# Kernel optimization log

Hardware: AMD Instinct MI355X
Metric: run time of the kernel (lower is better)

The kernel has to match this reference:

```python
import jax, jax.numpy as jnp
import numpy as np

# norse default LIF/LI parameters
DT = 0.001
TAU_SYN_INV = 200.0
TAU_MEM_INV = 100.0
V_TH = 1.0
ALPHA = 100.0        # SuperSpike surrogate slope (method='super', alpha=100)
T_ENC = 40           # ConstantCurrentLIFEncoder(40)
SCALE = 50.0

STATE_DIM = 256
ACTIONS = 18
HIDDEN = 128
BATCH = 1024

@jax.custom_vjp
def spike(x):
    return (x > 0).astype(x.dtype)

def _spike_fwd(x):
    return spike(x), x

def _spike_bwd(x, g):
    # SuperSpike surrogate: 1 / (alpha*|x| + 1)^2
    return (g / (ALPHA * jnp.abs(x) + 1.0) ** 2,)

spike.defvjp(_spike_fwd, _spike_bwd)

def encode(current):
    # constant-current LIF encoder: current [B, D] -> spikes [T_ENC, B, D]
    def step(v, _):
        v = v + DT * TAU_MEM_INV * (-v + current)   # v_leak = 0
        z = spike(v - V_TH)
        v = (1.0 - z) * v                            # reset to v_reset = 0
        return v, z
    _, zs = jax.lax.scan(step, jnp.zeros_like(current), None, length=T_ENC)
    return zs

def snn_forward(x, w_in, w_rec, w_actor, w_critic):
    # encode positive and negative rectified currents, concat on feature dim
    xs = jnp.concatenate([encode(jax.nn.relu(SCALE * x)),
                          encode(jax.nn.relu(-SCALE * x))], axis=2)  # [T, B, 2D]
    B = x.shape[0]
    H = w_in.shape[0]
    A = w_actor.shape[0]
    dt_ = x.dtype
    carry0 = (jnp.zeros((B, H), dt_), jnp.zeros((B, H), dt_), jnp.zeros((B, H), dt_),
              jnp.zeros((B, A), dt_), jnp.zeros((B, A), dt_),
              jnp.zeros((B, 1), dt_), jnp.zeros((B, 1), dt_))

    def step(carry, x_t):
        z, v, i, va, ia, vc, ic = carry
        # --- recurrent LIFCell (norse lif_step) ---
        v_dec = v + DT * TAU_MEM_INV * (-v + i)      # dv uses pre-decay i
        i_dec = i - DT * TAU_SYN_INV * i
        z_new = spike(v_dec - V_TH)
        v_new = (1.0 - z_new) * v_dec                # reset by z to v_reset = 0
        i_new = i_dec + x_t @ w_in.T + z @ w_rec.T   # recurrent input uses old z
        # --- LICell actor readout (norse li_step) ---
        va_new = va + DT * TAU_MEM_INV * (-va + ia)
        ia_new = ia - DT * TAU_SYN_INV * ia + z_new @ w_actor.T
        # --- LICell critic readout ---
        vc_new = vc + DT * TAU_MEM_INV * (-vc + ic)
        ic_new = ic - DT * TAU_SYN_INV * ic + z_new @ w_critic.T
        return (z_new, v_new, i_new, va_new, ia_new, vc_new, ic_new), (va_new, vc_new)

    _, (volt_a, volt_c) = jax.lax.scan(step, carry0, xs)
    m_a = jnp.max(volt_a, axis=0)                    # max over time
    m_c = jnp.max(volt_c, axis=0)
    return jax.nn.softmax(m_a, axis=1), m_c


def setup_inputs() -> dict:
    key = jax.random.key(0)
    k0, k1, k2, k3, k4 = jax.random.split(key, 5)
    in_feat = 2 * STATE_DIM
    x = jax.random.normal(k0, (BATCH, STATE_DIM), dtype=jnp.float32)
    # norse init: randn * sqrt(2 / input_size)
    w_in = jax.random.normal(k1, (HIDDEN, in_feat), dtype=jnp.float32) * np.sqrt(2.0 / in_feat)
    w_rec = jax.random.normal(k2, (HIDDEN, HIDDEN), dtype=jnp.float32) * np.sqrt(2.0 / HIDDEN)
    w_actor = jax.random.normal(k3, (ACTIONS, HIDDEN), dtype=jnp.float32) * np.sqrt(2.0 / HIDDEN)
    w_critic = jax.random.normal(k4, (1, HIDDEN), dtype=jnp.float32) * np.sqrt(2.0 / HIDDEN)
    return {"x": x, "w_in": w_in, "w_rec": w_rec, "w_actor": w_actor, "w_critic": w_critic}


def reference(x, w_in, w_rec, w_actor, w_critic):
    return snn_forward(x, w_in, w_rec, w_actor, w_critic)
```

## Files before the change

kernel.cpp:

```cpp
#include <hip/hip_runtime.h>
#include <hip/hip_bf16.h>
#include <stdint.h>

typedef __attribute__((ext_vector_type(4))) float f32x4;
typedef __attribute__((ext_vector_type(8))) short s16x8;
typedef __attribute__((ext_vector_type(4))) unsigned int u32x4;

#define OFF_I 2621440

__device__ __forceinline__ void lut_entry(uint32_t by, uint32_t* r) {
    uint32_t r0 = 0, r1 = 0, r2 = 0, r3 = 0;
    if (by & 1)   r0 |= 0x3F80u;
    if (by & 2)   r0 |= 0x3F800000u;
    if (by & 4)   r1 |= 0x3F80u;
    if (by & 8)   r1 |= 0x3F800000u;
    if (by & 16)  r2 |= 0x3F80u;
    if (by & 32)  r2 |= 0x3F800000u;
    if (by & 64)  r3 |= 0x3F80u;
    if (by & 128) r3 |= 0x3F800000u;
    r[0] = r0; r[1] = r1; r[2] = r2; r[3] = r3;
}

__global__ __launch_bounds__(256) void k_encode(const float* __restrict__ x,
                                                uint32_t* __restrict__ spk) {
    int gid  = blockIdx.x * 256 + threadIdx.x;
    int b    = gid >> 9;
    int f    = gid & 511;
    int lane = threadIdx.x & 63;
    float xv  = x[b * 256 + (f & 255)];
    float cur = (f < 256) ? fmaxf(50.f * xv, 0.f) : fmaxf(-50.f * xv, 0.f);
    int wbase = (f >> 6) << 1;
    float v = 0.f;
    for (int t = 0; t < 40; ++t) {
        v = v + 0.1f * (cur - v);
        bool z = (v - 1.0f) > 0.f;
        unsigned long long m = __ballot(z);
        if (z) v = 0.f;
        if (lane == 0)
            *(unsigned long long*)&spk[(size_t)(t * 1024 + b) * 16 + wbase] = m;
    }
}

__global__ __launch_bounds__(512, 1) void k_ingemm(const uint32_t* __restrict__ spk,
                                                   const float* __restrict__ w_in,
                                                   float* __restrict__ I) {
    __shared__ uint32_t lut[256][4];
    __shared__ float tile[16][128];
    const int tid = threadIdx.x;
    if (tid < 256) lut_entry(tid, lut[tid]);
    const int lane = tid & 63, wid = tid >> 6;
    const int fr = lane & 15, fo = lane >> 4;
    const int n0 = wid * 16;

#define LOADB(i) s16x8 bh##i, bl##i; { \
    const float* p = w_in + (n0 + fr) * 512 + (i) * 32 + fo * 8; \
    f32x4 fa = *(const f32x4*)p; f32x4 fb = *(const f32x4*)(p + 4); \
    _Pragma("unroll") for (int j = 0; j < 8; ++j) { \
        float f = (j < 4) ? fa[j] : fb[j - 4]; \
        __hip_bfloat16 hb = __float2bfloat16(f); \
        float r1 = f - __bfloat162float(hb); \
        __hip_bfloat16 lb = __float2bfloat16(r1); \
        bh##i[j] = (short)*(unsigned short*)&hb; \
        bl##i[j] = (short)*(unsigned short*)&lb; } }
    LOADB(0)  LOADB(1)  LOADB(2)  LOADB(3)  LOADB(4)  LOADB(5)  LOADB(6)  LOADB(7)
    LOADB(8)  LOADB(9)  LOADB(10) LOADB(11) LOADB(12) LOADB(13) LOADB(14) LOADB(15)
#undef LOADB
    asm volatile("" : "+v"(bh0), "+v"(bh1), "+v"(bh2),  "+v"(bh3),
                      "+v"(bh4), "+v"(bh5), "+v"(bh6),  "+v"(bh7),
                      "+v"(bh8), "+v"(bh9), "+v"(bh10), "+v"(bh11),
                      "+v"(bh12),"+v"(bh13),"+v"(bh14), "+v"(bh15));
    asm volatile("" : "+v"(bl0), "+v"(bl1), "+v"(bl2),  "+v"(bl3),
                      "+v"(bl4), "+v"(bl5), "+v"(bl6),  "+v"(bl7),
                      "+v"(bl8), "+v"(bl9), "+v"(bl10), "+v"(bl11),
                      "+v"(bl12),"+v"(bl13),"+v"(bl14), "+v"(bl15));
    __syncthreads();

    const int m0 = blockIdx.x * 160;
    const int srow = tid >> 5;
    const int sc0  = (tid & 31) * 4;
    for (int mt = 0; mt < 10; ++mt) {
        int mrow = m0 + mt * 16 + fr;
        u32x4 w0 = *(const u32x4*)&spk[mrow * 16];
        u32x4 w1 = *(const u32x4*)&spk[mrow * 16 + 4];
        u32x4 w2 = *(const u32x4*)&spk[mrow * 16 + 8];
        u32x4 w3 = *(const u32x4*)&spk[mrow * 16 + 12];
        f32x4 acc = (f32x4)0.f;
#define KSTEP(i, WSEL) { uint32_t by = ((WSEL) >> (fo * 8)) & 0xFFu; \
        union { u32x4 u; s16x8 v; } cv; cv.u = *(const u32x4*)lut[by]; \
        acc = __builtin_amdgcn_mfma_f32_16x16x32_bf16(cv.v, bh##i, acc, 0, 0, 0); \
        acc = __builtin_amdgcn_mfma_f32_16x16x32_bf16(cv.v, bl##i, acc, 0, 0, 0); }
        KSTEP(0,  w0[0]) KSTEP(1,  w0[1]) KSTEP(2,  w0[2]) KSTEP(3,  w0[3])
        KSTEP(4,  w1[0]) KSTEP(5,  w1[1]) KSTEP(6,  w1[2]) KSTEP(7,  w1[3])
        KSTEP(8,  w2[0]) KSTEP(9,  w2[1]) KSTEP(10, w2[2]) KSTEP(11, w2[3])
        KSTEP(12, w3[0]) KSTEP(13, w3[1]) KSTEP(14, w3[2]) KSTEP(15, w3[3])
#undef KSTEP
        __syncthreads();
#pragma unroll
        for (int r = 0; r < 4; ++r)
            tile[fo * 4 + r][n0 + fr] = acc[r];
        __syncthreads();
        f32x4 vv = *(const f32x4*)&tile[srow][sc0];
        *(f32x4*)&I[(size_t)(m0 + mt * 16 + srow) * 128 + sc0] = vv;
    }
}

__global__ __launch_bounds__(256, 1) void k_recur_ro(const float* __restrict__ I,
                                                     const float* __restrict__ w_rec,
                                                     const float* __restrict__ w_actor,
                                                     const float* __restrict__ w_critic,
                                                     float* __restrict__ out) {
    __shared__ uint32_t lut[256][4];
    __shared__ uint32_t zm[2][16][4];
    __shared__ float smax[16][20];
    const int tid = threadIdx.x;
    lut_entry(tid, lut[tid]);
    if (tid < 64) zm[0][tid >> 2][tid & 3] = 0;
    const int lane = tid & 63, w = tid >> 6;
    const int fr = lane & 15, fo = lane >> 4;
    const int n0 = w * 32;
    const int b0 = blockIdx.x * 16;

#define LOADW(ks, ni) s16x8 H##ks##ni, L##ks##ni, Q##ks##ni; { \
    const float* p = w_rec + (n0 + (ni) * 16 + fr) * 128 + (ks) * 32 + fo * 8; \
    _Pragma("unroll") for (int j = 0; j < 8; ++j) { \
        float f = p[j]; \
        __hip_bfloat16 hb = __float2bfloat16(f); \
        float r1 = f - __bfloat162float(hb); \
        __hip_bfloat16 lb = __float2bfloat16(r1); \
        float r2 = r1 - __bfloat162float(lb); \
        __hip_bfloat16 qb = __float2bfloat16(r2); \
        H##ks##ni[j] = (short)*(unsigned short*)&hb; \
        L##ks##ni[j] = (short)*(unsigned short*)&lb; \
        Q##ks##ni[j] = (short)*(unsigned short*)&qb; } }
    LOADW(0,0) LOADW(1,0) LOADW(2,0) LOADW(3,0)
    LOADW(0,1) LOADW(1,1) LOADW(2,1) LOADW(3,1)
#undef LOADW
    asm volatile("" : "+v"(H00), "+v"(H10), "+v"(H20), "+v"(H30),
                      "+v"(H01), "+v"(H11), "+v"(H21), "+v"(H31),
                      "+v"(L00), "+v"(L10), "+v"(L20), "+v"(L30));
    asm volatile("" : "+v"(L01), "+v"(L11), "+v"(L21), "+v"(L31),
                      "+v"(Q00), "+v"(Q10), "+v"(Q20), "+v"(Q30),
                      "+v"(Q01), "+v"(Q11), "+v"(Q21), "+v"(Q31));

    s16x8 rbh[4], rbl[4];
    const int a_ch = w * 16 + fr;
    const float* asrc = (a_ch < 18) ? (w_actor + a_ch * 128)
                       : ((a_ch == 18) ? w_critic : nullptr);
#pragma unroll
    for (int ks = 0; ks < 4; ++ks) {
#pragma unroll
        for (int j = 0; j < 8; ++j) {
            float f = asrc ? asrc[ks * 32 + fo * 8 + j] : 0.f;
            __hip_bfloat16 hb = __float2bfloat16(f);
            float r1 = f - __bfloat162float(hb);
            __hip_bfloat16 lb = __float2bfloat16(r1);
            rbh[ks][j] = (short)*(unsigned short*)&hb;
            rbl[ks][j] = (short)*(unsigned short*)&lb;
        }
    }
    f32x4 rva = (f32x4)0.f, ria = (f32x4)0.f, rma = (f32x4)(-1e30f);

    f32x4 v0 = (f32x4)0.f, v1 = (f32x4)0.f, c0 = (f32x4)0.f, c1 = (f32x4)0.f;

#define ILOAD(dst, t_, ni) { _Pragma("unroll") for (int r = 0; r < 4; ++r) \
    dst[r] = I[(size_t)((t_) * 1024 + b0 + fo * 4 + r) * 128 + n0 + (ni) * 16 + fr]; }
    f32x4 icur0, icur1;
    ILOAD(icur0, 0, 0) ILOAD(icur1, 0, 1)
    __syncthreads();

    for (int t = 0; t < 40; ++t) {
        int tn = (t < 39) ? t + 1 : 39;
        f32x4 inxt0, inxt1;
        ILOAD(inxt0, tn, 0) ILOAD(inxt1, tn, 1)

        u32x4 zw = *(const u32x4*)zm[t & 1][fr];
        union { u32x4 u; s16x8 v; } a0, a1, a2, a3;
        a0.u = *(const u32x4*)lut[(zw[0] >> (fo * 8)) & 0xFFu];
        a1.u = *(const u32x4*)lut[(zw[1] >> (fo * 8)) & 0xFFu];
        a2.u = *(const u32x4*)lut[(zw[2] >> (fo * 8)) & 0xFFu];
        a3.u = *(const u32x4*)lut[(zw[3] >> (fo * 8)) & 0xFFu];

        f32x4 r0 = (f32x4)0.f, r1 = (f32x4)0.f;
#define RECK(ks, av) \
        r0 = __builtin_amdgcn_mfma_f32_16x16x32_bf16(av, H##ks##0, r0, 0, 0, 0); \
        r0 = __builtin_amdgcn_mfma_f32_16x16x32_bf16(av, L##ks##0, r0, 0, 0, 0); \
        r0 = __builtin_amdgcn_mfma_f32_16x16x32_bf16(av, Q##ks##0, r0, 0, 0, 0); \
        r1 = __builtin_amdgcn_mfma_f32_16x16x32_bf16(av, H##ks##1, r1, 0, 0, 0); \
        r1 = __builtin_amdgcn_mfma_f32_16x16x32_bf16(av, L##ks##1, r1, 0, 0, 0); \
        r1 = __builtin_amdgcn_mfma_f32_16x16x32_bf16(av, Q##ks##1, r1, 0, 0, 0);
        RECK(0, a0.v) RECK(1, a1.v) RECK(2, a2.v) RECK(3, a3.v)
#undef RECK

        f32x4 vd0 = v0 + 0.1f * (c0 - v0);
        f32x4 vd1 = v1 + 0.1f * (c1 - v1);
        f32x4 id0 = c0 - 0.2f * c0;
        f32x4 id1 = c1 - 0.2f * c1;
        unsigned long long B00, B01, B02, B03, B10, B11, B12, B13;
        bool z;
        z = (vd0[0] - 1.0f) > 0.f; B00 = __ballot(z); if (z) vd0[0] = 0.f;
        z = (vd0[1] - 1.0f) > 0.f; B01 = __ballot(z); if (z) vd0[1] = 0.f;
        z = (vd0[2] - 1.0f) > 0.f; B02 = __ballot(z); if (z) vd0[2] = 0.f;
        z = (vd0[3] - 1.0f) > 0.f; B03 = __ballot(z); if (z) vd0[3] = 0.f;
        z = (vd1[0] - 1.0f) > 0.f; B10 = __ballot(z); if (z) vd1[0] = 0.f;
        z = (vd1[1] - 1.0f) > 0.f; B11 = __ballot(z); if (z) vd1[1] = 0.f;
        z = (vd1[2] - 1.0f) > 0.f; B12 = __ballot(z); if (z) vd1[2] = 0.f;
        z = (vd1[3] - 1.0f) > 0.f; B13 = __ballot(z); if (z) vd1[3] = 0.f;
        v0 = vd0; v1 = vd1;

        if (lane < 16) {
            int m = lane, rq = m & 3, sh = (m >> 2) * 16;
            unsigned long long s0 = (rq == 0) ? B00 : (rq == 1) ? B01 : (rq == 2) ? B02 : B03;
            unsigned long long s1 = (rq == 0) ? B10 : (rq == 1) ? B11 : (rq == 2) ? B12 : B13;
            uint32_t word = ((uint32_t)(s0 >> sh) & 0xFFFFu)
                          | (((uint32_t)(s1 >> sh) & 0xFFFFu) << 16);
            zm[(t & 1) ^ 1][m][w] = word;
        }

        c0 = (id0 + icur0) + r0;
        c1 = (id1 + icur1) + r1;
        icur0 = inxt0; icur1 = inxt1;
        __syncthreads();

        if (w < 2) {
            u32x4 zw2 = *(const u32x4*)zm[(t & 1) ^ 1][fr];
            f32x4 racc = (f32x4)0.f;
#pragma unroll
            for (int ks = 0; ks < 4; ++ks) {
                uint32_t by = (zw2[ks] >> (fo * 8)) & 0xFFu;
                union { u32x4 u; s16x8 v; } cv;
                cv.u = *(const u32x4*)lut[by];
                racc = __builtin_amdgcn_mfma_f32_16x16x32_bf16(cv.v, rbh[ks], racc, 0, 0, 0);
                racc = __builtin_amdgcn_mfma_f32_16x16x32_bf16(cv.v, rbl[ks], racc, 0, 0, 0);
            }
            f32x4 nva = rva + 0.1f * (ria - rva);
            ria = ria - 0.2f * ria + racc;
            rva = nva;
#pragma unroll
            for (int r = 0; r < 4; ++r)
                rma[r] = fmaxf(rma[r], nva[r]);
        }
    }
#undef ILOAD

    if (w == 0) {
#pragma unroll
        for (int r = 0; r < 4; ++r) smax[fo * 4 + r][fr] = rma[r];
    } else if (w == 1 && fr < 3) {
#pragma unroll
        for (int r = 0; r < 4; ++r) smax[fo * 4 + r][16 + fr] = rma[r];
    }
    __syncthreads();
    if (tid < 16) {
        int row = tid;
        float mx = -1e30f;
#pragma unroll
        for (int a2 = 0; a2 < 18; ++a2) mx = fmaxf(mx, smax[row][a2]);
        float s = 0.f;
#pragma unroll
        for (int a2 = 0; a2 < 18; ++a2) s += expf(smax[row][a2] - mx);
#pragma unroll
        for (int a2 = 0; a2 < 18; ++a2)
            out[(b0 + row) * 18 + a2] = expf(smax[row][a2] - mx) / s;
        out[18432 + b0 + row] = smax[row][18];
    }
}

extern "C" void kernel_launch(void* const* d_in, const int* in_sizes, int n_in,
                              void* d_out, int out_size, void* d_ws, size_t ws_size,
                              hipStream_t stream) {
    const float* x        = (const float*)d_in[0];
    const float* w_in     = (const float*)d_in[1];
    const float* w_rec    = (const float*)d_in[2];
    const float* w_actor  = (const float*)d_in[3];
    const float* w_critic = (const float*)d_in[4];
    float* out = (float*)d_out;
    char* ws = (char*)d_ws;
    uint32_t* spk = (uint32_t*)ws;
    float*    I   = (float*)(ws + OFF_I);

    hipLaunchKernelGGL(k_encode,   dim3(2048), dim3(256), 0, stream, x, spk);
    hipLaunchKernelGGL(k_ingemm,   dim3(256),  dim3(512), 0, stream, spk, w_in, I);
    hipLaunchKernelGGL(k_recur_ro, dim3(64),   dim3(256), 0, stream,
                       I, w_rec, w_actor, w_critic, out);
}
```

Baseline: 135.0 us.

## Split recurrent kernel across 8 waves with 16 hidden columns each

The recurrent LIF kernel now runs 512 threads per block, so each of eight waves owns 16 hidden neurons instead of 32. This halves the serial MFMA chain per wave on each time step. The spike bitmask moves to 16-bit words laid out so the existing 4x32-bit read still sees the same bytes. It adds barrier cost for more waves and relies on the new packing matching the old word layout.

```diff
diff --git a/kernel.cpp b/kernel.cpp
--- a/kernel.cpp
+++ b/kernel.cpp
@@ -104,24 +104,24 @@
     }
 }
 
-__global__ __launch_bounds__(256, 1) void k_recur_ro(const float* __restrict__ I,
+__global__ __launch_bounds__(512, 1) void k_recur_ro(const float* __restrict__ I,
                                                      const float* __restrict__ w_rec,
                                                      const float* __restrict__ w_actor,
                                                      const float* __restrict__ w_critic,
                                                      float* __restrict__ out) {
     __shared__ uint32_t lut[256][4];
-    __shared__ uint32_t zm[2][16][4];
+    __shared__ __align__(16) uint16_t zm16[2][16][8];
     __shared__ float smax[16][20];
     const int tid = threadIdx.x;
-    lut_entry(tid, lut[tid]);
-    if (tid < 64) zm[0][tid >> 2][tid & 3] = 0;
+    if (tid < 256) lut_entry(tid, lut[tid]);
+    if (tid < 128) ((uint16_t*)zm16)[tid] = 0;
     const int lane = tid & 63, w = tid >> 6;
     const int fr = lane & 15, fo = lane >> 4;
-    const int n0 = w * 32;
+    const int n0 = w * 16;
     const int b0 = blockIdx.x * 16;
 
-#define LOADW(ks, ni) s16x8 H##ks##ni, L##ks##ni, Q##ks##ni; { \
-    const float* p = w_rec + (n0 + (ni) * 16 + fr) * 128 + (ks) * 32 + fo * 8; \
+#define LOADW(ks) s16x8 H##ks, L##ks, Q##ks; { \
+    const float* p = w_rec + (n0 + fr) * 128 + (ks) * 32 + fo * 8; \
     _Pragma("unroll") for (int j = 0; j < 8; ++j) { \
         float f = p[j]; \
         __hip_bfloat16 hb = __float2bfloat16(f); \
@@ -129,23 +129,20 @@
         __hip_bfloat16 lb = __float2bfloat16(r1); \
         float r2 = r1 - __bfloat162float(lb); \
         __hip_bfloat16 qb = __float2bfloat16(r2); \
-        H##ks##ni[j] = (short)*(unsigned short*)&hb; \
-        L##ks##ni[j] = (short)*(unsigned short*)&lb; \
-        Q##ks##ni[j] = (short)*(unsigned short*)&qb; } }
-    LOADW(0,0) LOADW(1,0) LOADW(2,0) LOADW(3,0)
-    LOADW(0,1) LOADW(1,1) LOADW(2,1) LOADW(3,1)
+        H##ks[j] = (short)*(unsigned short*)&hb; \
+        L##ks[j] = (short)*(unsigned short*)&lb; \
+        Q##ks[j] = (short)*(unsigned short*)&qb; } }
+    LOADW(0) LOADW(1) LOADW(2) LOADW(3)
 #undef LOADW
-    asm volatile("" : "+v"(H00), "+v"(H10), "+v"(H20), "+v"(H30),
-                      "+v"(H01), "+v"(H11), "+v"(H21), "+v"(H31),
-                      "+v"(L00), "+v"(L10), "+v"(L20), "+v"(L30));
-    asm volatile("" : "+v"(L01), "+v"(L11), "+v"(L21), "+v"(L31),
-                      "+v"(Q00), "+v"(Q10), "+v"(Q20), "+v"(Q30),
-                      "+v"(Q01), "+v"(Q11), "+v"(Q21), "+v"(Q31));
+    asm volatile("" : "+v"(H0), "+v"(H1), "+v"(H2), "+v"(H3),
+                      "+v"(L0), "+v"(L1), "+v"(L2), "+v"(L3),
+                      "+v"(Q0), "+v"(Q1), "+v"(Q2), "+v"(Q3));
 
     s16x8 rbh[4], rbl[4];
     const int a_ch = w * 16 + fr;
-    const float* asrc = (a_ch < 18) ? (w_actor + a_ch * 128)
-                       : ((a_ch == 18) ? w_critic : nullptr);
+    const float* asrc = (w < 2)
+        ? ((a_ch < 18) ? (w_actor + a_ch * 128) : ((a_ch == 18) ? w_critic : nullptr))
+        : nullptr;
 #pragma unroll
     for (int ks = 0; ks < 4; ++ks) {
 #pragma unroll
@@ -160,69 +157,56 @@
     }
     f32x4 rva = (f32x4)0.f, ria = (f32x4)0.f, rma = (f32x4)(-1e30f);
 
-    f32x4 v0 = (f32x4)0.f, v1 = (f32x4)0.f, c0 = (f32x4)0.f, c1 = (f32x4)0.f;
-
-#define ILOAD(dst, t_, ni) { _Pragma("unroll") for (int r = 0; r < 4; ++r) \
-    dst[r] = I[(size_t)((t_) * 1024 + b0 + fo * 4 + r) * 128 + n0 + (ni) * 16 + fr]; }
-    f32x4 icur0, icur1;
-    ILOAD(icur0, 0, 0) ILOAD(icur1, 0, 1)
+    f32x4 v0 = (f32x4)0.f, c0 = (f32x4)0.f;
+
+#define ILOAD(dst, t_) { _Pragma("unroll") for (int r = 0; r < 4; ++r) \
+    dst[r] = I[(size_t)((t_) * 1024 + b0 + fo * 4 + r) * 128 + n0 + fr]; }
+    f32x4 icur;
+    ILOAD(icur, 0)
     __syncthreads();
 
     for (int t = 0; t < 40; ++t) {
         int tn = (t < 39) ? t + 1 : 39;
-        f32x4 inxt0, inxt1;
-        ILOAD(inxt0, tn, 0) ILOAD(inxt1, tn, 1)
-
-        u32x4 zw = *(const u32x4*)zm[t & 1][fr];
+        f32x4 inxt;
+        ILOAD(inxt, tn)
+
+        u32x4 zw = *(const u32x4*)zm16[t & 1][fr];
         union { u32x4 u; s16x8 v; } a0, a1, a2, a3;
         a0.u = *(const u32x4*)lut[(zw[0] >> (fo * 8)) & 0xFFu];
         a1.u = *(const u32x4*)lut[(zw[1] >> (fo * 8)) & 0xFFu];
         a2.u = *(const u32x4*)lut[(zw[2] >> (fo * 8)) & 0xFFu];
         a3.u = *(const u32x4*)lut[(zw[3] >> (fo * 8)) & 0xFFu];
 
-        f32x4 r0 = (f32x4)0.f, r1 = (f32x4)0.f;
+        f32x4 r0 = (f32x4)0.f;
 #define RECK(ks, av) \
-        r0 = __builtin_amdgcn_mfma_f32_16x16x32_bf16(av, H##ks##0, r0, 0, 0, 0); \
-        r0 = __builtin_amdgcn_mfma_f32_16x16x32_bf16(av, L##ks##0, r0, 0, 0, 0); \
-        r0 = __builtin_amdgcn_mfma_f32_16x16x32_bf16(av, Q##ks##0, r0, 0, 0, 0); \
-        r1 = __builtin_amdgcn_mfma_f32_16x16x32_bf16(av, H##ks##1, r1, 0, 0, 0); \
-        r1 = __builtin_amdgcn_mfma_f32_16x16x32_bf16(av, L##ks##1, r1, 0, 0, 0); \
-        r1 = __builtin_amdgcn_mfma_f32_16x16x32_bf16(av, Q##ks##1, r1, 0, 0, 0);
+        r0 = __builtin_amdgcn_mfma_f32_16x16x32_bf16(av, H##ks, r0, 0, 0, 0); \
+        r0 = __builtin_amdgcn_mfma_f32_16x16x32_bf16(av, L##ks, r0, 0, 0, 0); \
+        r0 = __builtin_amdgcn_mfma_f32_16x16x32_bf16(av, Q##ks, r0, 0, 0, 0);
         RECK(0, a0.v) RECK(1, a1.v) RECK(2, a2.v) RECK(3, a3.v)
 #undef RECK
 
-        f32x4 vd0 = v0 + 0.1f * (c0 - v0);
-        f32x4 vd1 = v1 + 0.1f * (c1 - v1);
-        f32x4 id0 = c0 - 0.2f * c0;
-        f32x4 id1 = c1 - 0.2f * c1;
-        unsigned long long B00, B01, B02, B03, B10, B11, B12, B13;
+        f32x4 vd = v0 + 0.1f * (c0 - v0);
+        f32x4 id = c0 - 0.2f * c0;
+        unsigned long long B0, B1, B2, B3;
         bool z;
-        z = (vd0[0] - 1.0f) > 0.f; B00 = __ballot(z); if (z) vd0[0] = 0.f;
-        z = (vd0[1] - 1.0f) > 0.f; B01 = __ballot(z); if (z) vd0[1] = 0.f;
-        z = (vd0[2] - 1.0f) > 0.f; B02 = __ballot(z); if (z) vd0[2] = 0.f;
-        z = (vd0[3] - 1.0f) > 0.f; B03 = __ballot(z); if (z) vd0[3] = 0.f;
-        z = (vd1[0] - 1.0f) > 0.f; B10 = __ballot(z); if (z) vd1[0] = 0.f;
-        z = (vd1[1] - 1.0f) > 0.f; B11 = __ballot(z); if (z) vd1[1] = 0.f;
-        z = (vd1[2] - 1.0f) > 0.f; B12 = __ballot(z); if (z) vd1[2] = 0.f;
-        z = (vd1[3] - 1.0f) > 0.f; B13 = __ballot(z); if (z) vd1[3] = 0.f;
-        v0 = vd0; v1 = vd1;
+        z = (vd[0] - 1.0f) > 0.f; B0 = __ballot(z); if (z) vd[0] = 0.f;
+        z = (vd[1] - 1.0f) > 0.f; B1 = __ballot(z); if (z) vd[1] = 0.f;
+        z = (vd[2] - 1.0f) > 0.f; B2 = __ballot(z); if (z) vd[2] = 0.f;
+        z = (vd[3] - 1.0f) > 0.f; B3 = __ballot(z); if (z) vd[3] = 0.f;
+        v0 = vd;
 
         if (lane < 16) {
             int m = lane, rq = m & 3, sh = (m >> 2) * 16;
-            unsigned long long s0 = (rq == 0) ? B00 : (rq == 1) ? B01 : (rq == 2) ? B02 : B03;
-            unsigned long long s1 = (rq == 0) ? B10 : (rq == 1) ? B11 : (rq == 2) ? B12 : B13;
-            uint32_t word = ((uint32_t)(s0 >> sh) & 0xFFFFu)
-                          | (((uint32_t)(s1 >> sh) & 0xFFFFu) << 16);
-            zm[(t & 1) ^ 1][m][w] = word;
+            unsigned long long s = (rq == 0) ? B0 : (rq == 1) ? B1 : (rq == 2) ? B2 : B3;
+            zm16[(t & 1) ^ 1][m][w] = (uint16_t)((s >> sh) & 0xFFFFu);
         }
 
-        c0 = (id0 + icur0) + r0;
-        c1 = (id1 + icur1) + r1;
-        icur0 = inxt0; icur1 = inxt1;
+        c0 = (id + icur) + r0;
+        icur = inxt;
         __syncthreads();
 
         if (w < 2) {
-            u32x4 zw2 = *(const u32x4*)zm[(t & 1) ^ 1][fr];
+            u32x4 zw2 = *(const u32x4*)zm16[(t & 1) ^ 1][fr];
             f32x4 racc = (f32x4)0.f;
 #pragma unroll
             for (int ks = 0; ks < 4; ++ks) {
@@ -280,6 +264,6 @@
 
     hipLaunchKernelGGL(k_encode,   dim3(2048), dim3(256), 0, stream, x, spk);
     hipLaunchKernelGGL(k_ingemm,   dim3(256),  dim3(512), 0, stream, spk, w_in, I);
-    hipLaunchKernelGGL(k_recur_ro, dim3(64),   dim3(256), 0, stream,
+    hipLaunchKernelGGL(k_recur_ro, dim3(64),   dim3(512), 0, stream,
                        I, w_rec, w_actor, w_critic, out);
 }
```

Measured after the change: 129.4 us. 4.2% less time.
